# Kernel tuning notes

Measured on AMD Instinct MI355X. Metric: run time of the kernel, lower is better.

The kernel has to match this reference:

```python
import jax, jax.numpy as jnp
import numpy as np

N = 100000
E = 1600000
IN_DIM = 128
OUT_DIM = 64


def setup_inputs() -> dict:
    key = jax.random.key(0)
    k_h, k_ei, k_ew, k_W, k_a = jax.random.split(key, 5)
    h = jax.random.normal(k_h, (N, IN_DIM), dtype=jnp.float32)
    edge_index = jax.random.randint(k_ei, (2, E), 0, N, dtype=jnp.int64)
    edge_weight = jax.random.uniform(k_ew, (E,), dtype=jnp.float32)
    # nn.Linear weights (Kaiming-uniform-ish scale)
    W = jax.random.uniform(k_W, (OUT_DIM, IN_DIM), dtype=jnp.float32,
                           minval=-1.0, maxval=1.0) / np.sqrt(IN_DIM)
    a = jax.random.uniform(k_a, (2 * OUT_DIM,), dtype=jnp.float32,
                           minval=-1.0, maxval=1.0) / np.sqrt(2 * OUT_DIM)
    return {"h": h, "edge_index": edge_index, "edge_weight": edge_weight,
            "W": W, "a": a}


def reference(h, edge_index, edge_weight, W, a):
    # Faithful translation of _GATConvSparse.forward (inference; dropout = identity).
    n = h.shape[0]
    src, dst = edge_index[0], edge_index[1]
    Wh = h @ W.T                                  # (N, out_dim)
    d = Wh.shape[1]
    # a(cat([Wh[src], Wh[dst]])) == Wh[src] @ a[:d] + Wh[dst] @ a[d:]
    alpha = Wh[src] @ a[:d] + Wh[dst] @ a[d:]     # (E,)
    alpha = alpha * edge_weight
    # Buggy-but-faithful 'softmax': segment-sum raw scores onto dst nodes...
    alpha_node = jax.ops.segment_sum(alpha, dst, num_segments=n)   # (N,)
    alpha_exp = jnp.exp(alpha_node - alpha_node.max())             # (N,)
    # ...then normalize per-edge exp(src) by sum of exp(src) over each dst segment.
    denom = jax.ops.segment_sum(alpha_exp[src], dst, num_segments=n)  # (N,)
    alpha_norm = alpha_exp[src] / (denom[dst] + 1e-9)              # (E,)
    out = jax.ops.segment_sum(alpha_norm[:, None] * Wh[src], dst,
                              num_segments=n)                      # (N, out_dim)
    return jax.nn.elu(out)
```

## Files before the change

### kernel.cpp

```cpp
#include <hip/hip_runtime.h>
#include <math.h>

#define Nn 100000
#define Ee 1600000
#define IND 128
#define OUTD 64
#define DPB 64
#define NB 1563
#define SCANCAP 1536
#define LCAP 1024
#define GB 1563
#define EB_BLOCKS 391
#define AFIX 1048576.0f

using bf16x8 = __attribute__((ext_vector_type(8))) short;
using f32x4 = __attribute__((ext_vector_type(4))) float;

__device__ __forceinline__ unsigned short f2bf(float f) {
    unsigned u = __float_as_uint(f);
    u = u + 0x7FFFu + ((u >> 16) & 1u);
    return (unsigned short)(u >> 16);
}
__device__ __forceinline__ float bf2f(unsigned short h) {
    return __uint_as_float(((unsigned)h) << 16);
}

__device__ __forceinline__ bool probe64(const void* __restrict__ ei) {
    const long long* p = (const long long*)ei;
    bool ok = true;
#pragma unroll
    for (int i = 0; i < 8; ++i) {
        long long v = p[i];
        ok = ok && (v >= 0 && v < Nn);
    }
    return ok;
}

__device__ __forceinline__ void load_edge(const void* ei, int e, bool is64,
                                          int& s, int& d) {
    if (is64) {
        const long long* p = (const long long*)ei;
        s = (int)p[e];
        d = (int)p[Ee + e];
    } else {
        const int* p = (const int*)ei;
        s = p[e];
        d = p[Ee + e];
    }
}

__device__ __forceinline__ int load_dst(const void* ei, int e, bool is64) {
    if (is64) return (int)((const long long*)ei)[Ee + e];
    return ((const int*)ei)[Ee + e];
}

__global__ __launch_bounds__(256) void k_fused(
    const float* __restrict__ h, const float* __restrict__ W,
    const float* __restrict__ a, unsigned short* __restrict__ Whb,
    float* __restrict__ s1, float* __restrict__ s2,
    const void* __restrict__ ei, int* __restrict__ bcount) {
    __shared__ unsigned short Ash[64][136];
    __shared__ unsigned short Wsh[64][136];
    __shared__ float al[2 * OUTD];
    int bid = blockIdx.x;
    int t = threadIdx.x;

    if (bid < GB) {
        int R = bid * 64;
        for (int i = t; i < 2048; i += 256) {
            float4 v = ((const float4*)W)[i];
            int r = i >> 5, c = (i & 31) << 2;
            unsigned lo = (unsigned)f2bf(v.x) | ((unsigned)f2bf(v.y) << 16);
            unsigned hi = (unsigned)f2bf(v.z) | ((unsigned)f2bf(v.w) << 16);
            *(uint2*)&Wsh[r][c] = make_uint2(lo, hi);
        }
        if (t < 32) ((float4*)al)[t] = ((const float4*)a)[t];
        for (int i = t; i < 2048; i += 256) {
            int r = i >> 5, c = (i & 31) << 2;
            int n = R + r;
            float4 v = make_float4(0.f, 0.f, 0.f, 0.f);
            if (n < Nn) v = ((const float4*)(h + (size_t)n * IND))[i & 31];
            unsigned lo = (unsigned)f2bf(v.x) | ((unsigned)f2bf(v.y) << 16);
            unsigned hi = (unsigned)f2bf(v.z) | ((unsigned)f2bf(v.w) << 16);
            *(uint2*)&Ash[r][c] = make_uint2(lo, hi);
        }
        __syncthreads();

        int w = t >> 6, l = t & 63;
        int li = l & 15, lg = l >> 4;
        f32x4 acc[4];
#pragma unroll
        for (int nt = 0; nt < 4; ++nt) acc[nt] = (f32x4){0.f, 0.f, 0.f, 0.f};
#pragma unroll
        for (int kk = 0; kk < 4; ++kk) {
            bf16x8 af = *(const bf16x8*)&Ash[w * 16 + li][kk * 32 + lg * 8];
#pragma unroll
            for (int nt = 0; nt < 4; ++nt) {
                bf16x8 bf = *(const bf16x8*)&Wsh[nt * 16 + li][kk * 32 + lg * 8];
                acc[nt] = __builtin_amdgcn_mfma_f32_16x16x32_bf16(af, bf,
                                                                  acc[nt],
                                                                  0, 0, 0);
            }
        }
        float p1[4] = {0.f, 0.f, 0.f, 0.f};
        float p2[4] = {0.f, 0.f, 0.f, 0.f};
#pragma unroll
        for (int nt = 0; nt < 4; ++nt) {
            float a1v = al[nt * 16 + li];
            float a2v = al[OUTD + nt * 16 + li];
#pragma unroll
            for (int r = 0; r < 4; ++r) {
                float v = acc[nt][r];
                p1[r] += v * a1v;
                p2[r] += v * a2v;
                int row = R + w * 16 + lg * 4 + r;
                if (row < Nn)
                    Whb[(size_t)row * OUTD + nt * 16 + li] = f2bf(v);
            }
        }
#pragma unroll
        for (int r = 0; r < 4; ++r) {
#pragma unroll
            for (int m = 1; m < 16; m <<= 1) {
                p1[r] += __shfl_xor(p1[r], m, 64);
                p2[r] += __shfl_xor(p2[r], m, 64);
            }
        }
        if (li < 4) {
            int row = R + w * 16 + lg * 4 + li;
            if (row < Nn) {
                s1[row] = p1[li];
                s2[row] = p2[li];
            }
        }
    } else {
        int* cnt = (int*)&Ash[0][0];
        for (int i = t; i < NB; i += 256) cnt[i] = 0;
        __syncthreads();
        bool is64 = probe64(ei);
        int base = (bid - GB) * 4096;
#pragma unroll
        for (int i = 0; i < 16; ++i) {
            int e = base + i * 256 + t;
            if (e < Ee) atomicAdd(&cnt[load_dst(ei, e, is64) >> 6], 1);
        }
        __syncthreads();
        for (int i = t; i < NB; i += 256) {
            int c = cnt[i];
            if (c) atomicAdd(bcount + i, c);
        }
    }
}

__global__ __launch_bounds__(1024) void k_scan(
    const int* __restrict__ bcount, int* __restrict__ boff,
    int* __restrict__ bcursor) {
    __shared__ int sd[1024];
    int t = threadIdx.x;
    int i0 = 2 * t, i1 = 2 * t + 1;
    int v0 = (i0 < NB) ? bcount[i0] : 0;
    int v1 = (i1 < NB) ? bcount[i1] : 0;
    int pair = v0 + v1;
    sd[t] = pair;
    __syncthreads();
    for (int off = 1; off < 1024; off <<= 1) {
        int add = (t >= off) ? sd[t - off] : 0;
        __syncthreads();
        sd[t] += add;
        __syncthreads();
    }
    int excl = sd[t] - pair;
    if (i0 < NB) {
        boff[i0] = excl;
        bcursor[i0] = excl;
    }
    if (i1 < NB) {
        boff[i1] = excl + v0;
        bcursor[i1] = excl + v0;
    }
    if (t == 0) boff[NB] = Ee;
}

__global__ __launch_bounds__(512) void k_binscatter(
    const void* __restrict__ ei, const float* __restrict__ ew,
    const float* __restrict__ s1, const float* __restrict__ s2,
    int* __restrict__ bcursor, uint2* __restrict__ bins) {
    __shared__ int cnt[NB];
    __shared__ int gbase[NB];
    for (int i = threadIdx.x; i < NB; i += 512) cnt[i] = 0;
    __syncthreads();
    bool is64 = probe64(ei);
    int base = blockIdx.x * 4096;
    unsigned rx[8];
    int ryi[8];
    int rb[8];
    int rk[8];
#pragma unroll
    for (int i = 0; i < 8; ++i) {
        int e = base + i * 512 + threadIdx.x;
        rb[i] = -1;
        rx[i] = 0;
        ryi[i] = 0;
        rk[i] = 0;
        if (e < Ee) {
            int s, d;
            load_edge(ei, e, is64, s, d);
            float alpha = (s1[s] + s2[d]) * ew[e];
            ryi[i] = (int)rintf(alpha * AFIX);
            int b = d >> 6;
            rb[i] = b;
            rk[i] = atomicAdd(&cnt[b], 1);
            rx[i] = (unsigned)s | ((unsigned)(d & 63) << 17);
        }
    }
    __syncthreads();
    for (int i = threadIdx.x; i < NB; i += 512) {
        int c = cnt[i];
        if (c) gbase[i] = atomicAdd(bcursor + i, c);
    }
    __syncthreads();
#pragma unroll
    for (int i = 0; i < 8; ++i) {
        if (rb[i] >= 0) {
            bins[gbase[rb[i]] + rk[i]] = make_uint2(rx[i], (unsigned)ryi[i]);
        }
    }
}

__global__ __launch_bounds__(256) void k_balpha(
    const uint2* __restrict__ bins, const int* __restrict__ boff,
    float* __restrict__ ae) {
    __shared__ int anl[DPB];
    int b = blockIdx.x;
    int t = threadIdx.x;
    if (t < DPB) anl[t] = 0;
    __syncthreads();
    int e0 = boff[b], e1 = boff[b + 1];
    for (int k = e0 + t; k < e1; k += 256) {
        uint2 r = bins[k];
        atomicAdd(&anl[r.x >> 17], (int)r.y);
    }
    __syncthreads();
    if (t < DPB) {
        int n = b * DPB + t;
        if (n < Nn) ae[n] = expf((float)anl[t] * (1.f / AFIX));
    }
}

#define AGG_BODY(NR)                                                         \
    {                                                                        \
        uint2 rr[NR];                                                        \
        unsigned ww[NR];                                                     \
        _Pragma("unroll") for (int j = 0; j < NR; ++j)                       \
            rr[j] = lrec[k + 2 * j + half];                                  \
        _Pragma("unroll") for (int j = 0; j < NR; ++j)                       \
            ww[j] = whb32[(rr[j].x & 0x1FFFF) * 32 + hl];                    \
        _Pragma("unroll") for (int j = 0; j < NR; ++j) {                     \
            float aa = __uint_as_float(rr[j].y);                             \
            acc.x += aa * __uint_as_float(ww[j] << 16);                      \
            acc.y += aa * __uint_as_float(ww[j] & 0xFFFF0000u);              \
            den += aa;                                                       \
        }                                                                    \
    }

__global__ __launch_bounds__(256, 8) void k_agg(
    const uint2* __restrict__ bins, const int* __restrict__ boff,
    const float* __restrict__ ae, const unsigned short* __restrict__ Whb,
    float* __restrict__ out) {
    __shared__ uint2 lrec[LCAP];
    __shared__ int cnt[32];
    __shared__ int sbase[32];
    int bid = blockIdx.x;
    int b = bid >> 1;
    int H = (bid & 1) << 5;
    int t = threadIdx.x;
    int lane = t & 63;
    int wave = t >> 6;
    int half = lane >> 5;
    int hl = lane & 31;
    int e0 = boff[b], e1 = boff[b + 1];
    int total = e1 - e0;
    const unsigned* whb32 = (const unsigned*)Whb;

    if (t < 32) cnt[t] = 0;
    __syncthreads();

    bool ok = (total <= SCANCAP);
    unsigned su[SCANCAP / 256];
    float sa[SCANCAP / 256];
    int srk[SCANCAP / 256];
    if (ok) {
#pragma unroll
        for (int i = 0; i < SCANCAP / 256; ++i) {
            int k = e0 + i * 256 + t;
            srk[i] = -1;
            if (k < e1) {
                uint2 r = bins[k];
                int lloc = (int)(r.x >> 17) - H;
                if ((unsigned)lloc < 32u) {
                    srk[i] = atomicAdd(&cnt[lloc], 1);
                    su[i] = r.x;
                    sa[i] = ae[r.x & 0x1FFFF];
                }
            }
        }
        __syncthreads();
        if (t < 32) {
            int v = cnt[t];
#pragma unroll
            for (int d = 1; d < 32; d <<= 1) {
                int u = __shfl_up(v, d, 64);
                if (t >= d) v += u;
            }
            sbase[t] = v;
        }
        __syncthreads();
        ok = (sbase[31] <= LCAP);
    }

    if (ok) {
#pragma unroll
        for (int i = 0; i < SCANCAP / 256; ++i) {
            if (srk[i] >= 0) {
                int lloc = (int)(su[i] >> 17) - H;
                int pos = sbase[lloc] - cnt[lloc] + srk[i];
                lrec[pos] = make_uint2(su[i], __float_as_uint(sa[i]));
            }
        }
        __syncthreads();

        for (int d = wave * 8; d < wave * 8 + 8; ++d) {
            int k1 = sbase[d];
            int k = k1 - cnt[d];
            float2 acc = make_float2(0.f, 0.f);
            float den = 0.f;
            for (; k + 15 < k1; k += 16) AGG_BODY(8);
            for (; k + 7 < k1; k += 8) AGG_BODY(4);
            for (; k + 1 < k1; k += 2) AGG_BODY(1);
            if (k < k1) {
                uint2 rA = lrec[k];
                unsigned wA = whb32[(rA.x & 0x1FFFF) * 32 + hl];
                float aA = half ? 0.f : __uint_as_float(rA.y);
                acc.x += aA * __uint_as_float(wA << 16);
                acc.y += aA * __uint_as_float(wA & 0xFFFF0000u);
                den += aA;
            }
            float ax = acc.x + __shfl_xor(acc.x, 32, 64);
            float ay = acc.y + __shfl_xor(acc.y, 32, 64);
            float dn = den + __shfl_xor(den, 32, 64);
            if (half == 0) {
                int n = b * DPB + H + d;
                if (n < Nn) {
                    float inv = 1.f / (dn + 1e-9f);
                    float vx = ax * inv;
                    float vy = ay * inv;
                    vx = vx > 0.f ? vx : expm1f(vx);
                    vy = vy > 0.f ? vy : expm1f(vy);
                    *(float2*)&out[(size_t)n * OUTD + hl * 2] =
                        make_float2(vx, vy);
                }
            }
        }
    } else {
        for (int j = 0; j < 8; ++j) {
            int dloc = H + wave * 8 + j;
            int n = b * DPB + dloc;
            if (n >= Nn) continue;
            float aa = 0.f, dd = 0.f;
            for (int k = e0; k < e1; ++k) {
                uint2 r = bins[k];
                if ((int)(r.x >> 17) == dloc) {
                    int s = r.x & 0x1FFFF;
                    float a = ae[s];
                    aa += a * bf2f(Whb[(size_t)s * OUTD + lane]);
                    dd += a;
                }
            }
            float v = aa / (dd + 1e-9f);
            v = v > 0.f ? v : expm1f(v);
            out[(size_t)n * OUTD + lane] = v;
        }
    }
}

extern "C" void kernel_launch(void* const* d_in, const int* in_sizes, int n_in,
                              void* d_out, int out_size, void* d_ws,
                              size_t ws_size, hipStream_t stream) {
    const float* h = (const float*)d_in[0];
    const void* ei = d_in[1];
    const float* ew = (const float*)d_in[2];
    const float* W = (const float*)d_in[3];
    const float* a = (const float*)d_in[4];
    float* out = (float*)d_out;

    unsigned short* Whb = (unsigned short*)d_ws;
    float* s1 = (float*)(Whb + (size_t)Nn * OUTD);
    float* s2 = s1 + Nn;
    float* ae = s2 + Nn;
    int* bcount = (int*)(ae + Nn);
    int* boff = bcount + 2048;
    int* bcursor = boff + 2048;
    uint2* bins = (uint2*)(bcursor + 2048);

    hipMemsetAsync(bcount, 0, 2048 * sizeof(int), stream);

    k_fused<<<GB + EB_BLOCKS, 256, 0, stream>>>(h, W, a, Whb, s1, s2, ei,
                                                bcount);
    k_scan<<<1, 1024, 0, stream>>>(bcount, boff, bcursor);
    k_binscatter<<<EB_BLOCKS, 512, 0, stream>>>(ei, ew, s1, s2, bcursor, bins);
    k_balpha<<<NB, 256, 0, stream>>>(bins, boff, ae);
    k_agg<<<2 * NB, 256, 0, stream>>>(bins, boff, ae, Whb, out);
}
```

Measured before the change: 118.7 us.

## Build per-destination CSR in bin pass and simplify aggregation kernel

Splits the packed bin records into separate source and alpha arrays, and turns the per-bucket alpha kernel into a local counting sort that writes per-destination offsets and source indices sorted by destination into the alpha array. The aggregation kernel then reads its CSR segment directly, which removes the shared-memory rescan, atomics and overflow fallback path. The cost is an extra read and scatter pass in the sort kernel, and ae is now fetched per edge from global memory inside the aggregation loop instead of being staged in LDS.

```diff
diff --git a/kernel.cpp b/kernel.cpp
--- a/kernel.cpp
+++ b/kernel.cpp
@@ -7,8 +7,6 @@
 #define OUTD 64
 #define DPB 64
 #define NB 1563
-#define SCANCAP 1536
-#define LCAP 1024
 #define GB 1563
 #define EB_BLOCKS 391
 #define AFIX 1048576.0f
@@ -184,7 +182,8 @@
 __global__ __launch_bounds__(512) void k_binscatter(
     const void* __restrict__ ei, const float* __restrict__ ew,
     const float* __restrict__ s1, const float* __restrict__ s2,
-    int* __restrict__ bcursor, uint2* __restrict__ bins) {
+    int* __restrict__ bcursor, unsigned* __restrict__ binsS,
+    int* __restrict__ binsA) {
     __shared__ int cnt[NB];
     __shared__ int gbase[NB];
     for (int i = threadIdx.x; i < NB; i += 512) cnt[i] = 0;
@@ -222,54 +221,81 @@
 #pragma unroll
     for (int i = 0; i < 8; ++i) {
         if (rb[i] >= 0) {
-            bins[gbase[rb[i]] + rk[i]] = make_uint2(rx[i], (unsigned)ryi[i]);
-        }
-    }
-}
-
-__global__ __launch_bounds__(256) void k_balpha(
-    const uint2* __restrict__ bins, const int* __restrict__ boff,
-    float* __restrict__ ae) {
+            int pos = gbase[rb[i]] + rk[i];
+            binsS[pos] = rx[i];
+            binsA[pos] = ryi[i];
+        }
+    }
+}
+
+__global__ __launch_bounds__(256) void k_bsort(
+    const unsigned* __restrict__ binsS, int* __restrict__ binsA,
+    const int* __restrict__ boff, float* __restrict__ ae,
+    int* __restrict__ doff) {
+    __shared__ int cnt[DPB];
     __shared__ int anl[DPB];
+    __shared__ int cur[DPB];
     int b = blockIdx.x;
     int t = threadIdx.x;
-    if (t < DPB) anl[t] = 0;
+    if (t < DPB) {
+        cnt[t] = 0;
+        anl[t] = 0;
+    }
     __syncthreads();
     int e0 = boff[b], e1 = boff[b + 1];
     for (int k = e0 + t; k < e1; k += 256) {
-        uint2 r = bins[k];
-        atomicAdd(&anl[r.x >> 17], (int)r.y);
+        unsigned u = binsS[k];
+        int al = binsA[k];
+        int dl = (int)(u >> 17);
+        atomicAdd(&cnt[dl], 1);
+        atomicAdd(&anl[dl], al);
     }
     __syncthreads();
     if (t < DPB) {
+        int v = cnt[t];
+#pragma unroll
+        for (int d = 1; d < DPB; d <<= 1) {
+            int u = __shfl_up(v, d, 64);
+            if (t >= d) v += u;
+        }
+        int seg0 = e0 + v - cnt[t];
+        cur[t] = seg0;
+        doff[b * DPB + t] = seg0;
         int n = b * DPB + t;
         if (n < Nn) ae[n] = expf((float)anl[t] * (1.f / AFIX));
     }
+    if (b == NB - 1 && t == 0) doff[NB * DPB] = e1;
+    __syncthreads();
+    for (int k = e0 + t; k < e1; k += 256) {
+        unsigned u = binsS[k];
+        int dl = (int)(u >> 17);
+        int pos = atomicAdd(&cur[dl], 1);
+        binsA[pos] = (int)(u & 0x1FFFFu);
+    }
 }
 
 #define AGG_BODY(NR)                                                         \
     {                                                                        \
-        uint2 rr[NR];                                                        \
+        int ss[NR];                                                          \
         unsigned ww[NR];                                                     \
+        float aa[NR];                                                        \
         _Pragma("unroll") for (int j = 0; j < NR; ++j)                       \
-            rr[j] = lrec[k + 2 * j + half];                                  \
-        _Pragma("unroll") for (int j = 0; j < NR; ++j)                       \
-            ww[j] = whb32[(rr[j].x & 0x1FFFF) * 32 + hl];                    \
+            ss[j] = srcs[k + 2 * j + half];                                  \
         _Pragma("unroll") for (int j = 0; j < NR; ++j) {                     \
-            float aa = __uint_as_float(rr[j].y);                             \
-            acc.x += aa * __uint_as_float(ww[j] << 16);                      \
-            acc.y += aa * __uint_as_float(ww[j] & 0xFFFF0000u);              \
-            den += aa;                                                       \
+            ww[j] = whb32[(unsigned)ss[j] * 32 + hl];                        \
+            aa[j] = ae[ss[j]];                                               \
         }                                                                    \
+        _Pragma("unroll") for (int j = 0; j < NR; ++j) {                     \
+            acc.x += aa[j] * __uint_as_float(ww[j] << 16);                   \
+            acc.y += aa[j] * __uint_as_float(ww[j] & 0xFFFF0000u);           \
+            den += aa[j];                                                    \
+        }                                                                    \
     }
 
 __global__ __launch_bounds__(256, 8) void k_agg(
-    const uint2* __restrict__ bins, const int* __restrict__ boff,
+    const int* __restrict__ srcs, const int* __restrict__ doff,
     const float* __restrict__ ae, const unsigned short* __restrict__ Whb,
     float* __restrict__ out) {
-    __shared__ uint2 lrec[LCAP];
-    __shared__ int cnt[32];
-    __shared__ int sbase[32];
     int bid = blockIdx.x;
     int b = bid >> 1;
     int H = (bid & 1) << 5;
@@ -278,107 +304,38 @@
     int wave = t >> 6;
     int half = lane >> 5;
     int hl = lane & 31;
-    int e0 = boff[b], e1 = boff[b + 1];
-    int total = e1 - e0;
     const unsigned* whb32 = (const unsigned*)Whb;
 
-    if (t < 32) cnt[t] = 0;
-    __syncthreads();
-
-    bool ok = (total <= SCANCAP);
-    unsigned su[SCANCAP / 256];
-    float sa[SCANCAP / 256];
-    int srk[SCANCAP / 256];
-    if (ok) {
-#pragma unroll
-        for (int i = 0; i < SCANCAP / 256; ++i) {
-            int k = e0 + i * 256 + t;
-            srk[i] = -1;
-            if (k < e1) {
-                uint2 r = bins[k];
-                int lloc = (int)(r.x >> 17) - H;
-                if ((unsigned)lloc < 32u) {
-                    srk[i] = atomicAdd(&cnt[lloc], 1);
-                    su[i] = r.x;
-                    sa[i] = ae[r.x & 0x1FFFF];
-                }
-            }
-        }
-        __syncthreads();
-        if (t < 32) {
-            int v = cnt[t];
-#pragma unroll
-            for (int d = 1; d < 32; d <<= 1) {
-                int u = __shfl_up(v, d, 64);
-                if (t >= d) v += u;
-            }
-            sbase[t] = v;
-        }
-        __syncthreads();
-        ok = (sbase[31] <= LCAP);
-    }
-
-    if (ok) {
-#pragma unroll
-        for (int i = 0; i < SCANCAP / 256; ++i) {
-            if (srk[i] >= 0) {
-                int lloc = (int)(su[i] >> 17) - H;
-                int pos = sbase[lloc] - cnt[lloc] + srk[i];
-                lrec[pos] = make_uint2(su[i], __float_as_uint(sa[i]));
-            }
-        }
-        __syncthreads();
-
-        for (int d = wave * 8; d < wave * 8 + 8; ++d) {
-            int k1 = sbase[d];
-            int k = k1 - cnt[d];
-            float2 acc = make_float2(0.f, 0.f);
-            float den = 0.f;
-            for (; k + 15 < k1; k += 16) AGG_BODY(8);
-            for (; k + 7 < k1; k += 8) AGG_BODY(4);
-            for (; k + 1 < k1; k += 2) AGG_BODY(1);
-            if (k < k1) {
-                uint2 rA = lrec[k];
-                unsigned wA = whb32[(rA.x & 0x1FFFF) * 32 + hl];
-                float aA = half ? 0.f : __uint_as_float(rA.y);
-                acc.x += aA * __uint_as_float(wA << 16);
-                acc.y += aA * __uint_as_float(wA & 0xFFFF0000u);
-                den += aA;
-            }
-            float ax = acc.x + __shfl_xor(acc.x, 32, 64);
-            float ay = acc.y + __shfl_xor(acc.y, 32, 64);
-            float dn = den + __shfl_xor(den, 32, 64);
-            if (half == 0) {
-                int n = b * DPB + H + d;
-                if (n < Nn) {
-                    float inv = 1.f / (dn + 1e-9f);
-                    float vx = ax * inv;
-                    float vy = ay * inv;
-                    vx = vx > 0.f ? vx : expm1f(vx);
-                    vy = vy > 0.f ? vy : expm1f(vy);
-                    *(float2*)&out[(size_t)n * OUTD + hl * 2] =
-                        make_float2(vx, vy);
-                }
-            }
-        }
-    } else {
-        for (int j = 0; j < 8; ++j) {
-            int dloc = H + wave * 8 + j;
-            int n = b * DPB + dloc;
-            if (n >= Nn) continue;
-            float aa = 0.f, dd = 0.f;
-            for (int k = e0; k < e1; ++k) {
-                uint2 r = bins[k];
-                if ((int)(r.x >> 17) == dloc) {
-                    int s = r.x & 0x1FFFF;
-                    float a = ae[s];
-                    aa += a * bf2f(Whb[(size_t)s * OUTD + lane]);
-                    dd += a;
-                }
-            }
-            float v = aa / (dd + 1e-9f);
-            v = v > 0.f ? v : expm1f(v);
-            out[(size_t)n * OUTD + lane] = v;
+#pragma unroll
+    for (int j = 0; j < 8; ++j) {
+        int d = H + wave * 8 + j;
+        int n = b * DPB + d;
+        if (n >= Nn) continue;
+        int k1 = doff[n + 1];
+        int k = doff[n];
+        float2 acc = make_float2(0.f, 0.f);
+        float den = 0.f;
+        for (; k + 15 < k1; k += 16) AGG_BODY(8);
+        for (; k + 7 < k1; k += 8) AGG_BODY(4);
+        for (; k + 1 < k1; k += 2) AGG_BODY(1);
+        if (k < k1) {
+            int s = srcs[k];
+            unsigned wA = whb32[(unsigned)s * 32 + hl];
+            float aA = half ? 0.f : ae[s];
+            acc.x += aA * __uint_as_float(wA << 16);
+            acc.y += aA * __uint_as_float(wA & 0xFFFF0000u);
+            den += aA;
+        }
+        float ax = acc.x + __shfl_xor(acc.x, 32, 64);
+        float ay = acc.y + __shfl_xor(acc.y, 32, 64);
+        float dn = den + __shfl_xor(den, 32, 64);
+        if (half == 0) {
+            float inv = 1.f / (dn + 1e-9f);
+            float vx = ax * inv;
+            float vy = ay * inv;
+            vx = vx > 0.f ? vx : expm1f(vx);
+            vy = vy > 0.f ? vy : expm1f(vy);
+            *(float2*)&out[(size_t)n * OUTD + hl * 2] = make_float2(vx, vy);
         }
     }
 }
@@ -400,14 +357,17 @@
     int* bcount = (int*)(ae + Nn);
     int* boff = bcount + 2048;
     int* bcursor = boff + 2048;
-    uint2* bins = (uint2*)(bcursor + 2048);
+    int* doff = bcursor + 2048;
+    unsigned* binsS = (unsigned*)(doff + 100048);
+    int* binsA = (int*)(binsS + Ee);
 
     hipMemsetAsync(bcount, 0, 2048 * sizeof(int), stream);
 
     k_fused<<<GB + EB_BLOCKS, 256, 0, stream>>>(h, W, a, Whb, s1, s2, ei,
                                                 bcount);
     k_scan<<<1, 1024, 0, stream>>>(bcount, boff, bcursor);
-    k_binscatter<<<EB_BLOCKS, 512, 0, stream>>>(ei, ew, s1, s2, bcursor, bins);
-    k_balpha<<<NB, 256, 0, stream>>>(bins, boff, ae);
-    k_agg<<<2 * NB, 256, 0, stream>>>(bins, boff, ae, Whb, out);
-}
+    k_binscatter<<<EB_BLOCKS, 512, 0, stream>>>(ei, ew, s1, s2, bcursor,
+                                                binsS, binsA);
+    k_bsort<<<NB, 256, 0, stream>>>(binsS, binsA, boff, ae, doff);
+    k_agg<<<2 * NB, 256, 0, stream>>>(binsA, doff, ae, Whb, out);
+}
```

After: 142.6 us. +20.2%, slower.
